# Kernel tuning notes

Hardware: AMD Instinct MI355X
Metric: run time of the kernel (lower is better)

## Reference

```python
import jax, jax.numpy as jnp
import numpy as np

NEG_SLOPE = 0.2  # PyG GATConv default negative_slope
H1, H2, H3 = 4, 4, 1
CH = 64  # hidden_dim (per-head out channels)
N_NODES = 50000
N_EDGES = 800000
IN_DIM = 128
N_CLASSES = 10


def _gat_layer(x, src, dst, n, W, a_src, a_dst, b, heads, ch):
    # x: [N, Fin], W: [Fin, heads*ch], a_src/a_dst: [heads, ch], b: [heads*ch]
    h = (x @ W).reshape(-1, heads, ch)              # [N, H, C]
    e_src = jnp.sum(h * a_src, axis=-1)             # [N, H]
    e_dst = jnp.sum(h * a_dst, axis=-1)             # [N, H]
    e = jax.nn.leaky_relu(e_src[src] + e_dst[dst], NEG_SLOPE)  # [E, H]
    # segment softmax over incoming edges of each dst node
    m = jax.ops.segment_max(e, dst, num_segments=n)            # [N, H]
    p = jnp.exp(e - m[dst])                                    # [E, H]
    s = jax.ops.segment_sum(p, dst, num_segments=n)            # [N, H]
    alpha = p / (s[dst] + 1e-16)                               # [E, H]
    out = jax.ops.segment_sum(alpha[:, :, None] * h[src], dst, num_segments=n)  # [N, H, C]
    return out.reshape(-1, heads * ch) + b


def setup_inputs() -> dict:
    key = jax.random.key(0)
    ks = jax.random.split(key, 16)

    def glorot(k, shape, fan_in):
        return jax.random.normal(k, shape, dtype=jnp.float32) * (1.0 / np.sqrt(fan_in))

    x = jax.random.normal(ks[0], (N_NODES, IN_DIM), dtype=jnp.float32)
    edge_index = jax.random.randint(ks[1], (2, N_EDGES), 0, N_NODES, dtype=jnp.int32)

    d1 = H1 * CH  # 256
    d2 = H2 * CH  # 256
    d3 = H3 * CH  # 64
    return {
        "x": x,
        "edge_index": edge_index,
        "W1": glorot(ks[2], (IN_DIM, d1), IN_DIM),
        "a1_src": glorot(ks[3], (H1, CH), CH),
        "a1_dst": glorot(ks[4], (H1, CH), CH),
        "b1": jnp.zeros((d1,), jnp.float32),
        "W2": glorot(ks[5], (d1, d2), d1),
        "a2_src": glorot(ks[6], (H2, CH), CH),
        "a2_dst": glorot(ks[7], (H2, CH), CH),
        "b2": jnp.zeros((d2,), jnp.float32),
        "W3": glorot(ks[8], (d2, d3), d2),
        "a3_src": glorot(ks[9], (H3, CH), CH),
        "a3_dst": glorot(ks[10], (H3, CH), CH),
        "b3": jnp.zeros((d3,), jnp.float32),
        "fc_W": glorot(ks[11], (CH, N_CLASSES), CH),
        "fc_b": jnp.zeros((N_CLASSES,), jnp.float32),
    }


def reference(x, edge_index, W1, a1_src, a1_dst, b1, W2, a2_src, a2_dst, b2,
              W3, a3_src, a3_dst, b3, fc_W, fc_b):
    n = x.shape[0]
    # PyG GATConv adds self-loops by default
    loops = jnp.arange(n, dtype=edge_index.dtype)
    src = jnp.concatenate([edge_index[0], loops])
    dst = jnp.concatenate([edge_index[1], loops])

    h = jax.nn.relu(_gat_layer(x, src, dst, n, W1, a1_src, a1_dst, b1, H1, CH))
    # dropout(p=0.3) is identity in eval mode
    h = jax.nn.relu(_gat_layer(h, src, dst, n, W2, a2_src, a2_dst, b2, H2, CH))
    h = jax.nn.relu(_gat_layer(h, src, dst, n, W3, a3_src, a3_dst, b3, H3, CH))
    return h @ fc_W + fc_b  # [N, num_classes]
```

## Files before the change

kernel.cpp:

```cpp
#include <hip/hip_runtime.h>

#define NN 50000
#define NE 800000
#define E2 (NE + NN)
#define IN_DIM 128
#define SCAN_B 196

typedef unsigned short u16;
typedef unsigned int u32;
typedef __attribute__((ext_vector_type(8))) short short8;
typedef __attribute__((ext_vector_type(4))) float f32x4;

__device__ inline u16 f2bf(float x) {
    u32 u = __float_as_uint(x);
    u32 r = (u + 0x7fff + ((u >> 16) & 1)) >> 16;
    return (u16)r;
}
__device__ inline float bf2f(u16 h) { return __uint_as_float(((u32)h) << 16); }

__global__ __launch_bounds__(256) void fill_i32(int* __restrict__ p, int v, int n) {
    int i = blockIdx.x * 256 + threadIdx.x;
    if (i < n) p[i] = v;
}

__global__ __launch_bounds__(256) void hist_dst(const int* __restrict__ ei, int* __restrict__ deg) {
    int e = blockIdx.x * 256 + threadIdx.x;
    if (e < NE) atomicAdd(&deg[ei[NE + e]], 1);
}

__global__ __launch_bounds__(256) void block_sums(const int* __restrict__ deg, int* __restrict__ bsum) {
    int b = blockIdx.x;
    int i = b * 256 + threadIdx.x;
    int v = (i < NN) ? deg[i] : 0;
#pragma unroll
    for (int off = 32; off; off >>= 1) v += __shfl_down(v, off);
    __shared__ int ws[4];
    if ((threadIdx.x & 63) == 0) ws[threadIdx.x >> 6] = v;
    __syncthreads();
    if (threadIdx.x == 0) bsum[b] = ws[0] + ws[1] + ws[2] + ws[3];
}

__global__ __launch_bounds__(256) void scan_bsums(const int* __restrict__ bsum, int* __restrict__ boff) {
    __shared__ int s[256];
    int t = threadIdx.x;
    int v = (t < SCAN_B) ? bsum[t] : 0;
    s[t] = v;
    __syncthreads();
    for (int off = 1; off < 256; off <<= 1) {
        int u = (t >= off) ? s[t - off] : 0;
        __syncthreads();
        s[t] += u;
        __syncthreads();
    }
    if (t < SCAN_B) boff[t] = s[t] - v;
}

__global__ __launch_bounds__(256) void scan_final(const int* __restrict__ deg,
                                                  const int* __restrict__ boff,
                                                  int* __restrict__ rowptr,
                                                  int* __restrict__ cursor) {
    int b = blockIdx.x;
    int t = threadIdx.x;
    int i = b * 256 + t;
    int v = (i < NN) ? deg[i] : 0;
    __shared__ int s[256];
    s[t] = v;
    __syncthreads();
    for (int off = 1; off < 256; off <<= 1) {
        int u = (t >= off) ? s[t - off] : 0;
        __syncthreads();
        s[t] += u;
        __syncthreads();
    }
    int excl = s[t] - v + boff[b];
    if (i < NN) { rowptr[i] = excl; cursor[i] = excl; }
    if (i == NN - 1) rowptr[NN] = excl + v;
}

__global__ __launch_bounds__(256) void scatter_csr(const int* __restrict__ ei,
                                                   int* __restrict__ cursor,
                                                   int* __restrict__ csr_src) {
    int e = blockIdx.x * 256 + threadIdx.x;
    if (e >= E2) return;
    int s, d;
    if (e < NE) { s = ei[e]; d = ei[NE + e]; } else { s = d = e - NE; }
    int pos = atomicAdd(&cursor[d], 1);
    csr_src[pos] = s;
}

__global__ __launch_bounds__(256) void xconv(const float* __restrict__ X,
                                             u16* __restrict__ Xh, u16* __restrict__ Xl,
                                             int total4) {
    int i = blockIdx.x * 256 + threadIdx.x;
    if (i >= total4) return;
    float4 v = reinterpret_cast<const float4*>(X)[i];
    ushort4 h, l;
    h.x = f2bf(v.x); l.x = f2bf(v.x - bf2f(h.x));
    h.y = f2bf(v.y); l.y = f2bf(v.y - bf2f(h.y));
    h.z = f2bf(v.z); l.z = f2bf(v.z - bf2f(h.z));
    h.w = f2bf(v.w); l.w = f2bf(v.w - bf2f(h.w));
    reinterpret_cast<ushort4*>(Xh)[i] = h;
    reinterpret_cast<ushort4*>(Xl)[i] = l;
}

__global__ __launch_bounds__(256) void wconv(const float* __restrict__ W,
                                             u16* __restrict__ Wh, u16* __restrict__ Wl,
                                             int K, int N) {
    int idx = blockIdx.x * 256 + threadIdx.x;
    if (idx >= K * N) return;
    int k = idx / N, n = idx - k * N;
    float w = W[idx];
    u16 hi = f2bf(w);
    Wh[(size_t)n * K + k] = hi;
    Wl[(size_t)n * K + k] = f2bf(w - bf2f(hi));
}

template<int BN, int KK>
__global__ __launch_bounds__(256) void gemm_mfma(const u16* __restrict__ Ah,
                                                 const u16* __restrict__ Al,
                                                 const u16* __restrict__ Wh,
                                                 const u16* __restrict__ Wl,
                                                 float* __restrict__ C,
                                                 int M, int N) {
    const int BM = 128, BK = 32, LDT = BK + 8;
    __shared__ u16 Ahs[BM][LDT], Als[BM][LDT];
    __shared__ u16 Bhs[BN][LDT], Bls[BN][LDT];
    const int FRN = BN / 32;
    int tid = threadIdx.x;
    int lane = tid & 63, wid = tid >> 6;
    int wm = wid >> 1, wn = wid & 1;
    int row0 = blockIdx.x * BM, col0 = blockIdx.y * BN;
    int l15 = lane & 15, lg = lane >> 4;

    f32x4 acc[4][FRN];
#pragma unroll
    for (int i = 0; i < 4; ++i)
#pragma unroll
        for (int j = 0; j < FRN; ++j) acc[i][j] = (f32x4){0.f, 0.f, 0.f, 0.f};

    for (int ko = 0; ko < KK; ko += BK) {
        __syncthreads();
#pragma unroll
        for (int cc = 0; cc < 2; ++cc) {
            int c = tid * 2 + cc;
            int r = c >> 2, sub = (c & 3) * 8;
            int gr = row0 + r;
            uint4 vh = make_uint4(0, 0, 0, 0), vl = vh;
            if (gr < M) {
                vh = *reinterpret_cast<const uint4*>(Ah + (size_t)gr * KK + ko + sub);
                vl = *reinterpret_cast<const uint4*>(Al + (size_t)gr * KK + ko + sub);
            }
            *reinterpret_cast<uint4*>(&Ahs[r][sub]) = vh;
            *reinterpret_cast<uint4*>(&Als[r][sub]) = vl;
        }
#pragma unroll
        for (int c = tid; c < BN * 4; c += 256) {
            int r = c >> 2, sub = (c & 3) * 8;
            int gc = col0 + r;
            uint4 vh = *reinterpret_cast<const uint4*>(Wh + (size_t)gc * KK + ko + sub);
            uint4 vl = *reinterpret_cast<const uint4*>(Wl + (size_t)gc * KK + ko + sub);
            *reinterpret_cast<uint4*>(&Bhs[r][sub]) = vh;
            *reinterpret_cast<uint4*>(&Bls[r][sub]) = vl;
        }
        __syncthreads();
        short8 ah[4], al[4], bh[FRN], bl[FRN];
#pragma unroll
        for (int i = 0; i < 4; ++i) {
            int r = wm * 64 + i * 16 + l15;
            ah[i] = *reinterpret_cast<const short8*>(&Ahs[r][lg * 8]);
            al[i] = *reinterpret_cast<const short8*>(&Als[r][lg * 8]);
        }
#pragma unroll
        for (int j = 0; j < FRN; ++j) {
            int cc = wn * (BN / 2) + j * 16 + l15;
            bh[j] = *reinterpret_cast<const short8*>(&Bhs[cc][lg * 8]);
            bl[j] = *reinterpret_cast<const short8*>(&Bls[cc][lg * 8]);
        }
#pragma unroll
        for (int i = 0; i < 4; ++i)
#pragma unroll
            for (int j = 0; j < FRN; ++j) {
                acc[i][j] = __builtin_amdgcn_mfma_f32_16x16x32_bf16(ah[i], bh[j], acc[i][j], 0, 0, 0);
                acc[i][j] = __builtin_amdgcn_mfma_f32_16x16x32_bf16(ah[i], bl[j], acc[i][j], 0, 0, 0);
                acc[i][j] = __builtin_amdgcn_mfma_f32_16x16x32_bf16(al[i], bh[j], acc[i][j], 0, 0, 0);
            }
    }
#pragma unroll
    for (int i = 0; i < 4; ++i)
#pragma unroll
        for (int rr = 0; rr < 4; ++rr) {
            int gr = row0 + wm * 64 + i * 16 + lg * 4 + rr;
            if (gr < M) {
#pragma unroll
                for (int j = 0; j < FRN; ++j)
                    C[(size_t)gr * N + col0 + wn * (BN / 2) + j * 16 + l15] = acc[i][j][rr];
            }
        }
}

__global__ void escore(const float* __restrict__ h, const float* __restrict__ as,
                       const float* __restrict__ ad, float* __restrict__ es,
                       float* __restrict__ ed, int H) {
    int n = blockIdx.x;
    int t = threadIdx.x;
    int D = blockDim.x;
    float hv = h[(size_t)n * D + t];
    float vs = hv * as[t];
    float vd = hv * ad[t];
#pragma unroll
    for (int off = 32; off; off >>= 1) {
        vs += __shfl_down(vs, off);
        vd += __shfl_down(vd, off);
    }
    if ((t & 63) == 0) {
        int head = t >> 6;
        es[n * H + head] = vs;
        ed[n * H + head] = vd;
    }
}

__global__ __launch_bounds__(256) void attn_csr(const int* __restrict__ rowptr,
                                                const int* __restrict__ csr_src,
                                                const float* __restrict__ es,
                                                const float* __restrict__ ed,
                                                float* __restrict__ ev,
                                                float* __restrict__ s_,
                                                int H, int logH) {
    int wid = threadIdx.x >> 6;
    int lane = threadIdx.x & 63;
    int n = blockIdx.x * 4 + wid;
    if (n >= NN) return;
    int head = lane & (H - 1);
    int j = lane >> logH;
    int JP = 64 >> logH;
    int start = rowptr[n], end = rowptr[n + 1];
    float edv = ed[n * H + head];
    float m = -1e30f;
    for (int i = start + j; i < end; i += JP) {
        int src = csr_src[i];
        float v = es[src * H + head] + edv;
        v = v > 0.f ? v : 0.2f * v;
        m = fmaxf(m, v);
    }
#pragma unroll
    for (int off = 1; off < 64; off <<= 1)
        if (off >= H) m = fmaxf(m, __shfl_xor(m, off));
    float sum = 0.f;
    for (int i = start + j; i < end; i += JP) {
        int src = csr_src[i];
        float v = es[src * H + head] + edv;
        v = v > 0.f ? v : 0.2f * v;
        float p = __expf(v - m);
        ev[i * H + head] = p;
        sum += p;
    }
#pragma unroll
    for (int off = 1; off < 64; off <<= 1)
        if (off >= H) sum += __shfl_xor(sum, off);
    if (lane < H) s_[n * H + lane] = sum;
}

template<int D, int H>
__global__ __launch_bounds__(256) void agg_csr4(const int* __restrict__ rowptr,
                                                const int* __restrict__ csr_src,
                                                const float* __restrict__ ev,
                                                const float* __restrict__ h,
                                                const float* __restrict__ s_,
                                                const float* __restrict__ b,
                                                u16* __restrict__ Oh,
                                                u16* __restrict__ Ol) {
    const int TPN = D / 4;
    const int NPB = 256 / TPN;
    int tid = threadIdx.x;
    int n = blockIdx.x * NPB + tid / TPN;
    if (n >= NN) return;
    int f0 = (tid % TPN) * 4;
    int head = f0 >> 6;
    int start = rowptr[n], end = rowptr[n + 1];
    float4 acc = make_float4(0.f, 0.f, 0.f, 0.f);
    int i = start;
    for (; i + 8 <= end; i += 8) {
        int s0 = csr_src[i + 0], s1 = csr_src[i + 1], s2 = csr_src[i + 2], s3 = csr_src[i + 3];
        int s4 = csr_src[i + 4], s5 = csr_src[i + 5], s6 = csr_src[i + 6], s7 = csr_src[i + 7];
        float p0 = ev[(i + 0) * H + head], p1 = ev[(i + 1) * H + head];
        float p2 = ev[(i + 2) * H + head], p3 = ev[(i + 3) * H + head];
        float p4 = ev[(i + 4) * H + head], p5 = ev[(i + 5) * H + head];
        float p6 = ev[(i + 6) * H + head], p7 = ev[(i + 7) * H + head];
        float4 h0 = *reinterpret_cast<const float4*>(h + (size_t)s0 * D + f0);
        float4 h1 = *reinterpret_cast<const float4*>(h + (size_t)s1 * D + f0);
        float4 h2 = *reinterpret_cast<const float4*>(h + (size_t)s2 * D + f0);
        float4 h3 = *reinterpret_cast<const float4*>(h + (size_t)s3 * D + f0);
        float4 h4 = *reinterpret_cast<const float4*>(h + (size_t)s4 * D + f0);
        float4 h5 = *reinterpret_cast<const float4*>(h + (size_t)s5 * D + f0);
        float4 h6 = *reinterpret_cast<const float4*>(h + (size_t)s6 * D + f0);
        float4 h7 = *reinterpret_cast<const float4*>(h + (size_t)s7 * D + f0);
        acc.x += p0 * h0.x + p1 * h1.x + p2 * h2.x + p3 * h3.x
               + p4 * h4.x + p5 * h5.x + p6 * h6.x + p7 * h7.x;
        acc.y += p0 * h0.y + p1 * h1.y + p2 * h2.y + p3 * h3.y
               + p4 * h4.y + p5 * h5.y + p6 * h6.y + p7 * h7.y;
        acc.z += p0 * h0.z + p1 * h1.z + p2 * h2.z + p3 * h3.z
               + p4 * h4.z + p5 * h5.z + p6 * h6.z + p7 * h7.z;
        acc.w += p0 * h0.w + p1 * h1.w + p2 * h2.w + p3 * h3.w
               + p4 * h4.w + p5 * h5.w + p6 * h6.w + p7 * h7.w;
    }
    for (; i < end; ++i) {
        int s0 = csr_src[i];
        float p0 = ev[i * H + head];
        float4 h0 = *reinterpret_cast<const float4*>(h + (size_t)s0 * D + f0);
        acc.x += p0 * h0.x; acc.y += p0 * h0.y; acc.z += p0 * h0.z; acc.w += p0 * h0.w;
    }
    float inv = 1.f / (s_[n * H + head] + 1e-16f);
    float4 bb = *reinterpret_cast<const float4*>(b + f0);
    float4 o;
    o.x = acc.x * inv + bb.x; o.y = acc.y * inv + bb.y;
    o.z = acc.z * inv + bb.z; o.w = acc.w * inv + bb.w;
    o.x = o.x > 0.f ? o.x : 0.f; o.y = o.y > 0.f ? o.y : 0.f;
    o.z = o.z > 0.f ? o.z : 0.f; o.w = o.w > 0.f ? o.w : 0.f;
    ushort4 hv, lv;
    hv.x = f2bf(o.x); lv.x = f2bf(o.x - bf2f(hv.x));
    hv.y = f2bf(o.y); lv.y = f2bf(o.y - bf2f(hv.y));
    hv.z = f2bf(o.z); lv.z = f2bf(o.z - bf2f(hv.z));
    hv.w = f2bf(o.w); lv.w = f2bf(o.w - bf2f(hv.w));
    *reinterpret_cast<ushort4*>(Oh + (size_t)n * D + f0) = hv;
    *reinterpret_cast<ushort4*>(Ol + (size_t)n * D + f0) = lv;
}

__global__ __launch_bounds__(256) void fc_kernel(const u16* __restrict__ Hh,
                                                 const u16* __restrict__ Hl,
                                                 const float* __restrict__ W,
                                                 const float* __restrict__ b,
                                                 float* __restrict__ out) {
    int idx = blockIdx.x * 256 + threadIdx.x;
    if (idx >= NN * 10) return;
    int n = idx / 10, j = idx - n * 10;
    float acc = b[j];
#pragma unroll
    for (int c = 0; c < 64; ++c) {
        float hv = bf2f(Hh[n * 64 + c]) + bf2f(Hl[n * 64 + c]);
        acc += hv * W[c * 10 + j];
    }
    out[idx] = acc;
}

extern "C" void kernel_launch(void* const* d_in, const int* in_sizes, int n_in,
                              void* d_out, int out_size, void* d_ws, size_t ws_size,
                              hipStream_t stream) {
    const float* x   = (const float*)d_in[0];
    const int*   ei  = (const int*)d_in[1];
    const float* W1  = (const float*)d_in[2];
    const float* a1s = (const float*)d_in[3];
    const float* a1d = (const float*)d_in[4];
    const float* b1  = (const float*)d_in[5];
    const float* W2  = (const float*)d_in[6];
    const float* a2s = (const float*)d_in[7];
    const float* a2d = (const float*)d_in[8];
    const float* b2  = (const float*)d_in[9];
    const float* W3  = (const float*)d_in[10];
    const float* a3s = (const float*)d_in[11];
    const float* a3d = (const float*)d_in[12];
    const float* b3  = (const float*)d_in[13];
    const float* fcW = (const float*)d_in[14];
    const float* fcb = (const float*)d_in[15];
    float* out = (float*)d_out;

    char* wp = (char*)d_ws;
    float* h   = (float*)wp;  wp += (size_t)NN * 256 * 4;
    u16* Ph    = (u16*)wp;    wp += (size_t)NN * 256 * 2;
    u16* Pl    = (u16*)wp;    wp += (size_t)NN * 256 * 2;
    u16* Xh    = (u16*)wp;    wp += (size_t)NN * 128 * 2;
    u16* Xl    = (u16*)wp;    wp += (size_t)NN * 128 * 2;
    float* EV  = (float*)Xh;
    float* ES  = (float*)wp;  wp += (size_t)NN * 4 * 4;
    float* ED  = (float*)wp;  wp += (size_t)NN * 4 * 4;
    float* S_  = (float*)wp;  wp += (size_t)NN * 4 * 4;
    u16* Wth   = (u16*)wp;    wp += 256 * 256 * 2;
    u16* Wtl   = (u16*)wp;    wp += 256 * 256 * 2;
    int* rowptr = (int*)wp;   wp += (NN + 1) * 4;
    int* csrsrc = (int*)wp;   wp += (size_t)E2 * 4;
    int* deg    = (int*)wp;   wp += NN * 4;
    int* bsum   = (int*)wp;   wp += 256 * 4;
    int* boff   = (int*)wp;   wp += 256 * 4;
    int* cursor = (int*)ES;

    fill_i32<<<(NN + 255) / 256, 256, 0, stream>>>(deg, 1, NN);
    hist_dst<<<(NE + 255) / 256, 256, 0, stream>>>(ei, deg);
    block_sums<<<SCAN_B, 256, 0, stream>>>(deg, bsum);
    scan_bsums<<<1, 256, 0, stream>>>(bsum, boff);
    scan_final<<<SCAN_B, 256, 0, stream>>>(deg, boff, rowptr, cursor);
    scatter_csr<<<(E2 + 255) / 256, 256, 0, stream>>>(ei, cursor, csrsrc);

    xconv<<<(NN * IN_DIM / 4 + 255) / 256, 256, 0, stream>>>(x, Xh, Xl, NN * IN_DIM / 4);

    const int MT = (NN + 127) / 128;

    wconv<<<(IN_DIM * 256 + 255) / 256, 256, 0, stream>>>(W1, Wth, Wtl, IN_DIM, 256);
    gemm_mfma<128, 128><<<dim3(MT, 2), 256, 0, stream>>>(Xh, Xl, Wth, Wtl, h, NN, 256);
    escore<<<NN, 256, 0, stream>>>(h, a1s, a1d, ES, ED, 4);
    attn_csr<<<(NN + 3) / 4, 256, 0, stream>>>(rowptr, csrsrc, ES, ED, EV, S_, 4, 2);
    agg_csr4<256, 4><<<(NN + 3) / 4, 256, 0, stream>>>(rowptr, csrsrc, EV, h, S_, b1, Ph, Pl);

    wconv<<<(256 * 256 + 255) / 256, 256, 0, stream>>>(W2, Wth, Wtl, 256, 256);
    gemm_mfma<128, 256><<<dim3(MT, 2), 256, 0, stream>>>(Ph, Pl, Wth, Wtl, h, NN, 256);
    escore<<<NN, 256, 0, stream>>>(h, a2s, a2d, ES, ED, 4);
    attn_csr<<<(NN + 3) / 4, 256, 0, stream>>>(rowptr, csrsrc, ES, ED, EV, S_, 4, 2);
    agg_csr4<256, 4><<<(NN + 3) / 4, 256, 0, stream>>>(rowptr, csrsrc, EV, h, S_, b2, Ph, Pl);

    wconv<<<(256 * 64 + 255) / 256, 256, 0, stream>>>(W3, Wth, Wtl, 256, 64);
    gemm_mfma<64, 256><<<dim3(MT, 1), 256, 0, stream>>>(Ph, Pl, Wth, Wtl, h, NN, 64);
    escore<<<NN, 64, 0, stream>>>(h, a3s, a3d, ES, ED, 1);
    attn_csr<<<(NN + 3) / 4, 256, 0, stream>>>(rowptr, csrsrc, ES, ED, EV, S_, 1, 0);
    agg_csr4<64, 1><<<(NN + 15) / 16, 256, 0, stream>>>(rowptr, csrsrc, EV, h, S_, b3, Ph, Pl);

    fc_kernel<<<(NN * 10 + 255) / 256, 256, 0, stream>>>(Ph, Pl, fcW, fcb, out);
}
```

Baseline: 630.2 us.

## Fuse attention softmax into aggregation and register-prefetch GEMM tiles

Removes the separate attn_csr kernel. Each aggregation thread group now computes the per-head max itself, recomputes exp scores on the fly and accumulates the softmax denominator alongside the weighted feature sum. This drops the EV and S_ edge buffers and their global round trips, at the cost of redundant exp and es gathers across feature lanes. The GEMM also prefetches the next K tile into registers while the current tile is computed, to overlap global loads with MFMA work.

New measurement: 609.3 us. 3.3% less time.

```diff
diff --git a/kernel.cpp b/kernel.cpp
--- a/kernel.cpp
+++ b/kernel.cpp
@@ -126,43 +126,61 @@
     __shared__ u16 Ahs[BM][LDT], Als[BM][LDT];
     __shared__ u16 Bhs[BN][LDT], Bls[BN][LDT];
     const int FRN = BN / 32;
+    const int NB = BN * 4 / 256;
     int tid = threadIdx.x;
     int lane = tid & 63, wid = tid >> 6;
     int wm = wid >> 1, wn = wid & 1;
     int row0 = blockIdx.x * BM, col0 = blockIdx.y * BN;
     int l15 = lane & 15, lg = lane >> 4;
 
-    f32x4 acc[4][FRN];
-#pragma unroll
-    for (int i = 0; i < 4; ++i)
-#pragma unroll
-        for (int j = 0; j < FRN; ++j) acc[i][j] = (f32x4){0.f, 0.f, 0.f, 0.f};
-
-    for (int ko = 0; ko < KK; ko += BK) {
-        __syncthreads();
-#pragma unroll
-        for (int cc = 0; cc < 2; ++cc) {
-            int c = tid * 2 + cc;
-            int r = c >> 2, sub = (c & 3) * 8;
-            int gr = row0 + r;
-            uint4 vh = make_uint4(0, 0, 0, 0), vl = vh;
-            if (gr < M) {
-                vh = *reinterpret_cast<const uint4*>(Ah + (size_t)gr * KK + ko + sub);
-                vl = *reinterpret_cast<const uint4*>(Al + (size_t)gr * KK + ko + sub);
-            }
-            *reinterpret_cast<uint4*>(&Ahs[r][sub]) = vh;
-            *reinterpret_cast<uint4*>(&Als[r][sub]) = vl;
-        }
-#pragma unroll
-        for (int c = tid; c < BN * 4; c += 256) {
+    int c0 = tid * 2;
+    int r_a = c0 >> 2, sub_a0 = (c0 & 3) * 8, sub_a1 = ((c0 + 1) & 3) * 8;
+    int gr_a = row0 + r_a;
+
+    uint4 avh[2], avl[2], bvh[NB], bvl[NB];
+    auto loadA = [&](int ko) {
+        if (gr_a < M) {
+            avh[0] = *reinterpret_cast<const uint4*>(Ah + (size_t)gr_a * KK + ko + sub_a0);
+            avl[0] = *reinterpret_cast<const uint4*>(Al + (size_t)gr_a * KK + ko + sub_a0);
+            avh[1] = *reinterpret_cast<const uint4*>(Ah + (size_t)gr_a * KK + ko + sub_a1);
+            avl[1] = *reinterpret_cast<const uint4*>(Al + (size_t)gr_a * KK + ko + sub_a1);
+        } else {
+            avh[0] = avh[1] = avl[0] = avl[1] = make_uint4(0, 0, 0, 0);
+        }
+    };
+    auto loadB = [&](int ko) {
+#pragma unroll
+        for (int q = 0; q < NB; ++q) {
+            int c = tid + q * 256;
             int r = c >> 2, sub = (c & 3) * 8;
             int gc = col0 + r;
-            uint4 vh = *reinterpret_cast<const uint4*>(Wh + (size_t)gc * KK + ko + sub);
-            uint4 vl = *reinterpret_cast<const uint4*>(Wl + (size_t)gc * KK + ko + sub);
-            *reinterpret_cast<uint4*>(&Bhs[r][sub]) = vh;
-            *reinterpret_cast<uint4*>(&Bls[r][sub]) = vl;
-        }
-        __syncthreads();
+            bvh[q] = *reinterpret_cast<const uint4*>(Wh + (size_t)gc * KK + ko + sub);
+            bvl[q] = *reinterpret_cast<const uint4*>(Wl + (size_t)gc * KK + ko + sub);
+        }
+    };
+
+    f32x4 acc[4][FRN];
+#pragma unroll
+    for (int i = 0; i < 4; ++i)
+#pragma unroll
+        for (int j = 0; j < FRN; ++j) acc[i][j] = (f32x4){0.f, 0.f, 0.f, 0.f};
+
+    loadA(0); loadB(0);
+    for (int ko = 0; ko < KK; ko += BK) {
+        __syncthreads();
+        *reinterpret_cast<uint4*>(&Ahs[r_a][sub_a0]) = avh[0];
+        *reinterpret_cast<uint4*>(&Als[r_a][sub_a0]) = avl[0];
+        *reinterpret_cast<uint4*>(&Ahs[r_a][sub_a1]) = avh[1];
+        *reinterpret_cast<uint4*>(&Als[r_a][sub_a1]) = avl[1];
+#pragma unroll
+        for (int q = 0; q < NB; ++q) {
+            int c = tid + q * 256;
+            int r = c >> 2, sub = (c & 3) * 8;
+            *reinterpret_cast<uint4*>(&Bhs[r][sub]) = bvh[q];
+            *reinterpret_cast<uint4*>(&Bls[r][sub]) = bvl[q];
+        }
+        __syncthreads();
+        if (ko + BK < KK) { loadA(ko + BK); loadB(ko + BK); }
         short8 ah[4], al[4], bh[FRN], bl[FRN];
 #pragma unroll
         for (int i = 0; i < 4; ++i) {
@@ -219,73 +237,62 @@
     }
 }
 
-__global__ __launch_bounds__(256) void attn_csr(const int* __restrict__ rowptr,
-                                                const int* __restrict__ csr_src,
-                                                const float* __restrict__ es,
-                                                const float* __restrict__ ed,
-                                                float* __restrict__ ev,
-                                                float* __restrict__ s_,
-                                                int H, int logH) {
-    int wid = threadIdx.x >> 6;
-    int lane = threadIdx.x & 63;
-    int n = blockIdx.x * 4 + wid;
-    if (n >= NN) return;
-    int head = lane & (H - 1);
-    int j = lane >> logH;
-    int JP = 64 >> logH;
-    int start = rowptr[n], end = rowptr[n + 1];
-    float edv = ed[n * H + head];
-    float m = -1e30f;
-    for (int i = start + j; i < end; i += JP) {
-        int src = csr_src[i];
-        float v = es[src * H + head] + edv;
-        v = v > 0.f ? v : 0.2f * v;
-        m = fmaxf(m, v);
-    }
-#pragma unroll
-    for (int off = 1; off < 64; off <<= 1)
-        if (off >= H) m = fmaxf(m, __shfl_xor(m, off));
-    float sum = 0.f;
-    for (int i = start + j; i < end; i += JP) {
-        int src = csr_src[i];
-        float v = es[src * H + head] + edv;
-        v = v > 0.f ? v : 0.2f * v;
-        float p = __expf(v - m);
-        ev[i * H + head] = p;
-        sum += p;
-    }
-#pragma unroll
-    for (int off = 1; off < 64; off <<= 1)
-        if (off >= H) sum += __shfl_xor(sum, off);
-    if (lane < H) s_[n * H + lane] = sum;
-}
-
 template<int D, int H>
-__global__ __launch_bounds__(256) void agg_csr4(const int* __restrict__ rowptr,
-                                                const int* __restrict__ csr_src,
-                                                const float* __restrict__ ev,
-                                                const float* __restrict__ h,
-                                                const float* __restrict__ s_,
-                                                const float* __restrict__ b,
-                                                u16* __restrict__ Oh,
-                                                u16* __restrict__ Ol) {
+__global__ __launch_bounds__(256) void agg_fused(const int* __restrict__ rowptr,
+                                                 const int* __restrict__ csr_src,
+                                                 const float* __restrict__ es,
+                                                 const float* __restrict__ ed,
+                                                 const float* __restrict__ h,
+                                                 const float* __restrict__ b,
+                                                 u16* __restrict__ Oh,
+                                                 u16* __restrict__ Ol) {
     const int TPN = D / 4;
     const int NPB = 256 / TPN;
+    const int logH = (H == 4) ? 2 : 0;
     int tid = threadIdx.x;
     int n = blockIdx.x * NPB + tid / TPN;
     if (n >= NN) return;
-    int f0 = (tid % TPN) * 4;
-    int head = f0 >> 6;
+    int gl = tid % TPN;
     int start = rowptr[n], end = rowptr[n + 1];
+
+    int headA = gl & (H - 1);
+    const int JP = TPN >> logH;
+    float edvA = ed[n * H + headA];
+    float m = -1e30f;
+    for (int i = start + (gl >> logH); i < end; i += JP) {
+        int src = csr_src[i];
+        float v = es[src * H + headA] + edvA;
+        v = v > 0.f ? v : 0.2f * v;
+        m = fmaxf(m, v);
+    }
+#pragma unroll
+    for (int off = H; off < TPN; off <<= 1)
+        m = fmaxf(m, __shfl_xor(m, off));
+
+    int f0 = gl * 4;
+    int hb = f0 >> 6;
+    float mB;
+    if (D == 256) mB = __shfl(m, hb);
+    else          mB = m;
+    float edv = ed[n * H + hb];
+    float sump = 0.f;
     float4 acc = make_float4(0.f, 0.f, 0.f, 0.f);
     int i = start;
     for (; i + 8 <= end; i += 8) {
         int s0 = csr_src[i + 0], s1 = csr_src[i + 1], s2 = csr_src[i + 2], s3 = csr_src[i + 3];
         int s4 = csr_src[i + 4], s5 = csr_src[i + 5], s6 = csr_src[i + 6], s7 = csr_src[i + 7];
-        float p0 = ev[(i + 0) * H + head], p1 = ev[(i + 1) * H + head];
-        float p2 = ev[(i + 2) * H + head], p3 = ev[(i + 3) * H + head];
-        float p4 = ev[(i + 4) * H + head], p5 = ev[(i + 5) * H + head];
-        float p6 = ev[(i + 6) * H + head], p7 = ev[(i + 7) * H + head];
+        float v0 = es[s0 * H + hb] + edv, v1 = es[s1 * H + hb] + edv;
+        float v2 = es[s2 * H + hb] + edv, v3 = es[s3 * H + hb] + edv;
+        float v4 = es[s4 * H + hb] + edv, v5 = es[s5 * H + hb] + edv;
+        float v6 = es[s6 * H + hb] + edv, v7 = es[s7 * H + hb] + edv;
+        v0 = v0 > 0.f ? v0 : 0.2f * v0; v1 = v1 > 0.f ? v1 : 0.2f * v1;
+        v2 = v2 > 0.f ? v2 : 0.2f * v2; v3 = v3 > 0.f ? v3 : 0.2f * v3;
+        v4 = v4 > 0.f ? v4 : 0.2f * v4; v5 = v5 > 0.f ? v5 : 0.2f * v5;
+        v6 = v6 > 0.f ? v6 : 0.2f * v6; v7 = v7 > 0.f ? v7 : 0.2f * v7;
+        float p0 = __expf(v0 - mB), p1 = __expf(v1 - mB);
+        float p2 = __expf(v2 - mB), p3 = __expf(v3 - mB);
+        float p4 = __expf(v4 - mB), p5 = __expf(v5 - mB);
+        float p6 = __expf(v6 - mB), p7 = __expf(v7 - mB);
         float4 h0 = *reinterpret_cast<const float4*>(h + (size_t)s0 * D + f0);
         float4 h1 = *reinterpret_cast<const float4*>(h + (size_t)s1 * D + f0);
         float4 h2 = *reinterpret_cast<const float4*>(h + (size_t)s2 * D + f0);
@@ -302,14 +309,18 @@
                + p4 * h4.z + p5 * h5.z + p6 * h6.z + p7 * h7.z;
         acc.w += p0 * h0.w + p1 * h1.w + p2 * h2.w + p3 * h3.w
                + p4 * h4.w + p5 * h5.w + p6 * h6.w + p7 * h7.w;
+        sump += p0 + p1 + p2 + p3 + p4 + p5 + p6 + p7;
     }
     for (; i < end; ++i) {
         int s0 = csr_src[i];
-        float p0 = ev[i * H + head];
+        float v = es[s0 * H + hb] + edv;
+        v = v > 0.f ? v : 0.2f * v;
+        float p = __expf(v - mB);
         float4 h0 = *reinterpret_cast<const float4*>(h + (size_t)s0 * D + f0);
-        acc.x += p0 * h0.x; acc.y += p0 * h0.y; acc.z += p0 * h0.z; acc.w += p0 * h0.w;
-    }
-    float inv = 1.f / (s_[n * H + head] + 1e-16f);
+        acc.x += p * h0.x; acc.y += p * h0.y; acc.z += p * h0.z; acc.w += p * h0.w;
+        sump += p;
+    }
+    float inv = 1.f / (sump + 1e-16f);
     float4 bb = *reinterpret_cast<const float4*>(b + f0);
     float4 o;
     o.x = acc.x * inv + bb.x; o.y = acc.y * inv + bb.y;
@@ -369,10 +380,8 @@
     u16* Pl    = (u16*)wp;    wp += (size_t)NN * 256 * 2;
     u16* Xh    = (u16*)wp;    wp += (size_t)NN * 128 * 2;
     u16* Xl    = (u16*)wp;    wp += (size_t)NN * 128 * 2;
-    float* EV  = (float*)Xh;
     float* ES  = (float*)wp;  wp += (size_t)NN * 4 * 4;
     float* ED  = (float*)wp;  wp += (size_t)NN * 4 * 4;
-    float* S_  = (float*)wp;  wp += (size_t)NN * 4 * 4;
     u16* Wth   = (u16*)wp;    wp += 256 * 256 * 2;
     u16* Wtl   = (u16*)wp;    wp += 256 * 256 * 2;
     int* rowptr = (int*)wp;   wp += (NN + 1) * 4;
@@ -396,20 +405,17 @@
     wconv<<<(IN_DIM * 256 + 255) / 256, 256, 0, stream>>>(W1, Wth, Wtl, IN_DIM, 256);
     gemm_mfma<128, 128><<<dim3(MT, 2), 256, 0, stream>>>(Xh, Xl, Wth, Wtl, h, NN, 256);
     escore<<<NN, 256, 0, stream>>>(h, a1s, a1d, ES, ED, 4);
-    attn_csr<<<(NN + 3) / 4, 256, 0, stream>>>(rowptr, csrsrc, ES, ED, EV, S_, 4, 2);
-    agg_csr4<256, 4><<<(NN + 3) / 4, 256, 0, stream>>>(rowptr, csrsrc, EV, h, S_, b1, Ph, Pl);
+    agg_fused<256, 4><<<(NN + 3) / 4, 256, 0, stream>>>(rowptr, csrsrc, ES, ED, h, b1, Ph, Pl);
 
     wconv<<<(256 * 256 + 255) / 256, 256, 0, stream>>>(W2, Wth, Wtl, 256, 256);
     gemm_mfma<128, 256><<<dim3(MT, 2), 256, 0, stream>>>(Ph, Pl, Wth, Wtl, h, NN, 256);
     escore<<<NN, 256, 0, stream>>>(h, a2s, a2d, ES, ED, 4);
-    attn_csr<<<(NN + 3) / 4, 256, 0, stream>>>(rowptr, csrsrc, ES, ED, EV, S_, 4, 2);
-    agg_csr4<256, 4><<<(NN + 3) / 4, 256, 0, stream>>>(rowptr, csrsrc, EV, h, S_, b2, Ph, Pl);
+    agg_fused<256, 4><<<(NN + 3) / 4, 256, 0, stream>>>(rowptr, csrsrc, ES, ED, h, b2, Ph, Pl);
 
     wconv<<<(256 * 64 + 255) / 256, 256, 0, stream>>>(W3, Wth, Wtl, 256, 64);
     gemm_mfma<64, 256><<<dim3(MT, 1), 256, 0, stream>>>(Ph, Pl, Wth, Wtl, h, NN, 64);
     escore<<<NN, 64, 0, stream>>>(h, a3s, a3d, ES, ED, 1);
-    attn_csr<<<(NN + 3) / 4, 256, 0, stream>>>(rowptr, csrsrc, ES, ED, EV, S_, 1, 0);
-    agg_csr4<64, 1><<<(NN + 15) / 16, 256, 0, stream>>>(rowptr, csrsrc, EV, h, S_, b3, Ph, Pl);
+    agg_fused<64, 1><<<(NN + 15) / 16, 256, 0, stream>>>(rowptr, csrsrc, ES, ED, h, b3, Ph, Pl);
 
     fc_kernel<<<(NN * 10 + 255) / 256, 256, 0, stream>>>(Ph, Pl, fcW, fcb, out);
 }
```
